# Kernel tuning notes

Measured on AMD Instinct MI355X. Metric: run time of the kernel, lower is better.

## Reference

```python
import jax, jax.numpy as jnp
import numpy as np


def setup_inputs() -> dict:
    key = jax.random.key(0)
    k1, k2, k3 = jax.random.split(key, 3)
    N, C, W = 32, 64, 4096
    F, WW = 128, 64
    x = jax.random.normal(k1, (N, C, W), dtype=jnp.float32)
    w = jax.random.normal(k2, (F, C, WW), dtype=jnp.float32)
    b = jax.random.normal(k3, (F,), dtype=jnp.float32)
    return {"x": x, "w": w, "b": b}


def reference(x, w, b):
    # FFT-based 1D cross-correlation (the original loops over N, F, C; here batched).
    # x: [N, C, W], w: [F, C, WW], b: [F]
    N, C, W = x.shape
    F, _, WW = w.shape
    pad = 0  # module's padding kwarg
    fftsize = 1 << int(np.ceil(np.log2(W + 2 * pad + WW - 1)))  # next_power2
    out_W = W + 2 * pad - WW + 1
    # rfft of zero-padded signals and filters
    xfft = jnp.fft.rfft(x, n=fftsize, axis=-1)          # [N, C, K]
    wfft = jnp.fft.rfft(w, n=fftsize, axis=-1)          # [F, C, K]
    # cross-correlation: multiply by conj of filter spectrum, sum over channels
    offt = jnp.einsum('nck,fck->nfk', xfft, jnp.conj(wfft))  # [N, F, K]
    out = jnp.fft.irfft(offt, n=fftsize, axis=-1)[..., :out_W]  # real part, first out_W samples
    return out + b[None, :, None]
```

## Files before the change

kernel.cpp:

```cpp
#include <hip/hip_runtime.h>


#define C_TOT    64
#define F_TOT    128
#define KW       64
#define OUT_W    4033
#define W_IN     4096
#define N_BATCH  32
#define T_BLK    256
#define XROWS    320
#define XSTR     40
#define WROW     40
#define TRS      260
#define CHUNK_SH 10240

typedef __attribute__((ext_vector_type(8))) short  short8;
typedef __attribute__((ext_vector_type(4))) float  floatx4;

__device__ inline unsigned short f32_to_bf16(float f) {
  unsigned int u = __float_as_uint(f);
  u += 0x7FFF + ((u >> 16) & 1);
  return (unsigned short)(u >> 16);
}

__device__ inline void async16(const unsigned short* g, unsigned short* l) {
  __builtin_amdgcn_global_load_lds(
      (const __attribute__((address_space(1))) unsigned int*)g,
      (__attribute__((address_space(3))) unsigned int*)l, 16, 0, 0);
}

__global__ __launch_bounds__(256) void conv1d_prep(
    const float* __restrict__ w, unsigned short* __restrict__ wsw) {
  int j = blockIdx.x * 256 + threadIdx.x;
  if (j < 64 * 2 * 128 * 8) {
    int c4  = (j & 7) * 4;
    int f   = (j >> 3) & 127;
    int tap = (j >> 10) & 1;
    int gi  = j >> 11;
    int k   = (gi & 15) + 32 * ((gi >> 4) & 1) + 16 * tap;
    int cg0 = (gi >> 5) * 32 + c4;
    const float* src = w + ((size_t)f * C_TOT + cg0) * KW + k;
    ushort4 o;
    o.x = f32_to_bf16(src[0 * KW]);
    o.y = f32_to_bf16(src[1 * KW]);
    o.z = f32_to_bf16(src[2 * KW]);
    o.w = f32_to_bf16(src[3 * KW]);
    *(ushort4*)&wsw[((size_t)(gi * 2 + tap) * 128 + f) * WROW + c4] = o;
  }
}

__global__ __launch_bounds__(256, 2) void conv1d_mfma(
    const float* __restrict__ x, const unsigned short* __restrict__ wsw,
    const float* __restrict__ b, float* __restrict__ out) {
  __shared__ union SM {
    unsigned short xt[XROWS * XSTR];
    float tr[32 * TRS];
  } sm;
  __shared__ unsigned short bls[2][CHUNK_SH];

  const int tid  = threadIdx.x;
  const int lane = tid & 63;
  const int q    = lane >> 4;
  const int col  = lane & 15;
  const int wv   = tid >> 6;
  const int n    = blockIdx.y;
  const int t0   = blockIdx.x * T_BLK;
  const int fh2  = wv & 1;
  const int th   = wv >> 1;

  const float* xrowb = x + (size_t)n * C_TOT * W_IN;

  floatx4 acc[8][4];
#pragma unroll
  for (int ms = 0; ms < 8; ++ms)
#pragma unroll
    for (int ft = 0; ft < 4; ++ft) acc[ms][ft] = (floatx4)0.0f;

#define STAGE_W(gi_, p_)                                                       \
  {                                                                            \
    const unsigned short* wb = wsw + (size_t)(gi_) * CHUNK_SH;                 \
    _Pragma("unroll")                                                          \
    for (int s = 0; s < 5; ++s) {                                              \
      int off = (s * 256 + tid) * 8;                                           \
      async16(wb + off, &bls[p_][off]);                                        \
    }                                                                          \
  }

#define STAGE_X(hc_)                                                           \
  {                                                                            \
    _Pragma("unroll")                                                          \
    for (int r = 0; r < 10; ++r) {                                             \
      int ti = (r % 5) * 64 + (tid & 63);                                      \
      int cl = ((r / 5) * 4 + (tid >> 6)) * 4;                                 \
      int gt = t0 + ti;                                                        \
      const float* src = xrowb + (size_t)((hc_) * 32 + cl) * W_IN + gt;        \
      float4 v = {0.f, 0.f, 0.f, 0.f};                                         \
      if (gt < W_IN) {                                                         \
        v.x = src[0];                                                          \
        v.y = src[W_IN];                                                       \
        v.z = src[2 * W_IN];                                                   \
        v.w = src[3 * W_IN];                                                   \
      }                                                                        \
      ushort4 o;                                                               \
      o.x = f32_to_bf16(v.x); o.y = f32_to_bf16(v.y);                          \
      o.z = f32_to_bf16(v.z); o.w = f32_to_bf16(v.w);                          \
      *(ushort4*)&sm.xt[ti * XSTR + cl] = o;                                   \
    }                                                                          \
  }

  STAGE_W(0, 0)
  STAGE_X(0)
  __syncthreads();

  for (int gi = 0; gi < 64; ++gi) {
    const int p = gi & 1;
    if (gi + 1 < 64) STAGE_W(gi + 1, p ^ 1)

    const int k1 = (gi & 15) + 32 * ((gi >> 4) & 1);
    const unsigned short* ap = &sm.xt[(128 * th + col + k1) * XSTR + q * 8];
    const unsigned short* bp = &bls[p][(fh2 * 64 + col) * WROW + q * 8];

    short8 A[9];
#pragma unroll
    for (int jj = 0; jj < 9; ++jj)
      A[jj] = *(const short8*)&ap[jj * 16 * XSTR];

#pragma unroll
    for (int tap = 0; tap < 2; ++tap) {
#pragma unroll
      for (int ft = 0; ft < 4; ++ft) {
        const short8 B = *(const short8*)&bp[(tap * 128 + ft * 16) * WROW];
#pragma unroll
        for (int ms = 0; ms < 8; ++ms)
          acc[ms][ft] = __builtin_amdgcn_mfma_f32_16x16x32_bf16(
              A[ms + tap], B, acc[ms][ft], 0, 0, 0);
      }
    }
    __syncthreads();
    if (gi == 31) {
      STAGE_X(1)
      __syncthreads();
    }
  }

  const int fs_w  = fh2 * 16 + col;
  const int fs_r  = tid >> 3;
  const int seg   = tid & 7;
  const int f_r   = (fs_r >> 4) * 64 + (fs_r & 15);
  const size_t ob = ((size_t)n * F_TOT) * OUT_W;

#pragma unroll
  for (int j = 0; j < 4; ++j) {
#pragma unroll
    for (int ms = 0; ms < 8; ++ms) {
      float4 vv;
      vv.x = acc[ms][j][0];
      vv.y = acc[ms][j][1];
      vv.z = acc[ms][j][2];
      vv.w = acc[ms][j][3];
      int tl = 128 * th + 16 * ms + 4 * q;
      *(float4*)&sm.tr[fs_w * TRS + tl] = vv;
    }
    __syncthreads();
    const int f = f_r + 16 * j;
    const float bias = b[f];
    const size_t obf = ob + (size_t)f * OUT_W;
#pragma unroll
    for (int j2 = 0; j2 < 8; ++j2) {
      int tl = seg * 4 + 32 * j2;
      float4 vv = *(const float4*)&sm.tr[fs_r * TRS + tl];
      vv.x += bias; vv.y += bias; vv.z += bias; vv.w += bias;
      int t = t0 + tl;
      if (t + 3 < OUT_W) {
        *(float4*)&out[obf + t] = vv;
      } else {
        float e[4] = {vv.x, vv.y, vv.z, vv.w};
#pragma unroll
        for (int u = 0; u < 4; ++u)
          if (t + u < OUT_W) out[obf + t + u] = e[u];
      }
    }
    __syncthreads();
  }
}

extern "C" void kernel_launch(void* const* d_in, const int* in_sizes, int n_in,
                              void* d_out, int out_size, void* d_ws, size_t ws_size,
                              hipStream_t stream) {
  const float* x = (const float*)d_in[0];
  const float* w = (const float*)d_in[1];
  const float* b = (const float*)d_in[2];
  float* out = (float*)d_out;

  unsigned short* wsw = (unsigned short*)d_ws;

  conv1d_prep<<<512, 256, 0, stream>>>(w, wsw);

  dim3 grid((OUT_W + T_BLK - 1) / T_BLK, N_BATCH);
  conv1d_mfma<<<grid, 256, 0, stream>>>(x, wsw, b, out);
}
```

Before: 194.7 us.

## Load pre-swizzled weight fragments directly from global into registers, drop LDS staging

```diff
diff --git a/kernel.cpp b/kernel.cpp
--- a/kernel.cpp
+++ b/kernel.cpp
@@ -10,9 +10,7 @@
 #define T_BLK    256
 #define XROWS    320
 #define XSTR     40
-#define WROW     40
 #define TRS      260
-#define CHUNK_SH 10240
 
 typedef __attribute__((ext_vector_type(8))) short  short8;
 typedef __attribute__((ext_vector_type(4))) float  floatx4;
@@ -23,29 +21,27 @@
   return (unsigned short)(u >> 16);
 }
 
-__device__ inline void async16(const unsigned short* g, unsigned short* l) {
-  __builtin_amdgcn_global_load_lds(
-      (const __attribute__((address_space(1))) unsigned int*)g,
-      (__attribute__((address_space(3))) unsigned int*)l, 16, 0, 0);
-}
-
 __global__ __launch_bounds__(256) void conv1d_prep(
     const float* __restrict__ w, unsigned short* __restrict__ wsw) {
   int j = blockIdx.x * 256 + threadIdx.x;
-  if (j < 64 * 2 * 128 * 8) {
-    int c4  = (j & 7) * 4;
-    int f   = (j >> 3) & 127;
+  if (j < 131072) {
+    int e4  = (j & 1) * 4;
+    int col = (j >> 1) & 15;
+    int q   = (j >> 5) & 3;
+    int ft  = (j >> 7) & 3;
+    int fh2 = (j >> 9) & 1;
     int tap = (j >> 10) & 1;
     int gi  = j >> 11;
     int k   = (gi & 15) + 32 * ((gi >> 4) & 1) + 16 * tap;
-    int cg0 = (gi >> 5) * 32 + c4;
-    const float* src = w + ((size_t)f * C_TOT + cg0) * KW + k;
+    int f   = fh2 * 64 + ft * 16 + col;
+    int c0  = (gi >> 5) * 32 + q * 8 + e4;
+    const float* src = w + ((size_t)f * C_TOT + c0) * KW + k;
     ushort4 o;
     o.x = f32_to_bf16(src[0 * KW]);
     o.y = f32_to_bf16(src[1 * KW]);
     o.z = f32_to_bf16(src[2 * KW]);
     o.w = f32_to_bf16(src[3 * KW]);
-    *(ushort4*)&wsw[((size_t)(gi * 2 + tap) * 128 + f) * WROW + c4] = o;
+    *(ushort4*)&wsw[(size_t)j * 4] = o;
   }
 }
 
@@ -56,7 +52,6 @@
     unsigned short xt[XROWS * XSTR];
     float tr[32 * TRS];
   } sm;
-  __shared__ unsigned short bls[2][CHUNK_SH];
 
   const int tid  = threadIdx.x;
   const int lane = tid & 63;
@@ -69,22 +64,13 @@
   const int th   = wv >> 1;
 
   const float* xrowb = x + (size_t)n * C_TOT * W_IN;
+  const short8* wf = (const short8*)wsw;
 
   floatx4 acc[8][4];
 #pragma unroll
   for (int ms = 0; ms < 8; ++ms)
 #pragma unroll
     for (int ft = 0; ft < 4; ++ft) acc[ms][ft] = (floatx4)0.0f;
-
-#define STAGE_W(gi_, p_)                                                       \
-  {                                                                            \
-    const unsigned short* wb = wsw + (size_t)(gi_) * CHUNK_SH;                 \
-    _Pragma("unroll")                                                          \
-    for (int s = 0; s < 5; ++s) {                                              \
-      int off = (s * 256 + tid) * 8;                                           \
-      async16(wb + off, &bls[p_][off]);                                        \
-    }                                                                          \
-  }
 
 #define STAGE_X(hc_)                                                           \
   {                                                                            \
@@ -108,40 +94,57 @@
     }                                                                          \
   }
 
-  STAGE_W(0, 0)
+#define BFRAG(gi_, tap_, ft_) \
+  wf[(size_t)(((gi_) * 2 + (tap_)) * 2 + fh2) * 256 + (ft_) * 64 + lane]
+
+#define BODY(gi_, Bt0_, Bn_)                                                   \
+  {                                                                            \
+    const int k1 = ((gi_) & 15) + 32 * (((gi_) >> 4) & 1);                     \
+    short8 Bt1[4];                                                             \
+    _Pragma("unroll")                                                          \
+    for (int ft = 0; ft < 4; ++ft) Bt1[ft] = BFRAG(gi_, 1, ft);                \
+    const unsigned short* ap = &sm.xt[(128 * th + col + k1) * XSTR + q * 8];   \
+    short8 A[9];                                                               \
+    _Pragma("unroll")                                                          \
+    for (int jj = 0; jj < 9; ++jj)                                             \
+      A[jj] = *(const short8*)&ap[jj * 16 * XSTR];                             \
+    if ((gi_) + 1 < 64) {                                                      \
+      _Pragma("unroll")                                                        \
+      for (int ft = 0; ft < 4; ++ft) Bn_[ft] = BFRAG((gi_) + 1, 0, ft);        \
+    }                                                                          \
+    __builtin_amdgcn_s_setprio(1);                                             \
+    _Pragma("unroll")                                                          \
+    for (int ft = 0; ft < 4; ++ft)                                             \
+      _Pragma("unroll")                                                        \
+      for (int ms = 0; ms < 8; ++ms)                                           \
+        acc[ms][ft] = __builtin_amdgcn_mfma_f32_16x16x32_bf16(                 \
+            A[ms], Bt0_[ft], acc[ms][ft], 0, 0, 0);                            \
+    _Pragma("unroll")                                                          \
+    for (int ft = 0; ft < 4; ++ft)                                             \
+      _Pragma("unroll")                                                        \
+      for (int ms = 0; ms < 8; ++ms)                                           \
+        acc[ms][ft] = __builtin_amdgcn_mfma_f32_16x16x32_bf16(                 \
+            A[ms + 1], Bt1[ft], acc[ms][ft], 0, 0, 0);                         \
+    __builtin_amdgcn_s_setprio(0);                                             \
+  }
+
   STAGE_X(0)
+  short8 B0[4], B1[4];
+#pragma unroll
+  for (int ft = 0; ft < 4; ++ft) B0[ft] = BFRAG(0, 0, ft);
   __syncthreads();
 
-  for (int gi = 0; gi < 64; ++gi) {
-    const int p = gi & 1;
-    if (gi + 1 < 64) STAGE_W(gi + 1, p ^ 1)
-
-    const int k1 = (gi & 15) + 32 * ((gi >> 4) & 1);
-    const unsigned short* ap = &sm.xt[(128 * th + col + k1) * XSTR + q * 8];
-    const unsigned short* bp = &bls[p][(fh2 * 64 + col) * WROW + q * 8];
-
-    short8 A[9];
-#pragma unroll
-    for (int jj = 0; jj < 9; ++jj)
-      A[jj] = *(const short8*)&ap[jj * 16 * XSTR];
-
-#pragma unroll
-    for (int tap = 0; tap < 2; ++tap) {
-#pragma unroll
-      for (int ft = 0; ft < 4; ++ft) {
-        const short8 B = *(const short8*)&bp[(tap * 128 + ft * 16) * WROW];
-#pragma unroll
-        for (int ms = 0; ms < 8; ++ms)
-          acc[ms][ft] = __builtin_amdgcn_mfma_f32_16x16x32_bf16(
-              A[ms + tap], B, acc[ms][ft], 0, 0, 0);
-      }
-    }
-    __syncthreads();
-    if (gi == 31) {
+  for (int g2 = 0; g2 < 32; ++g2) {
+    const int gi = 2 * g2;
+    BODY(gi, B0, B1)
+    BODY(gi + 1, B1, B0)
+    if (gi + 1 == 31) {
+      __syncthreads();
       STAGE_X(1)
       __syncthreads();
     }
   }
+  __syncthreads();
 
   const int fs_w  = fh2 * 16 + col;
   const int fs_r  = tid >> 3;
```

Measured after the change: 188.8 us. 1.03x faster.

## Switch to 32x32x16 MFMA with register-direct weight fragments and full-channel x staging

Applied to the files above, without the earlier changes.

```diff
diff --git a/kernel.cpp b/kernel.cpp
--- a/kernel.cpp
+++ b/kernel.cpp
@@ -9,13 +9,11 @@
 #define N_BATCH  32
 #define T_BLK    256
 #define XROWS    320
-#define XSTR     40
-#define WROW     40
+#define XSTR     72
 #define TRS      260
-#define CHUNK_SH 10240
 
-typedef __attribute__((ext_vector_type(8))) short  short8;
-typedef __attribute__((ext_vector_type(4))) float  floatx4;
+typedef __attribute__((ext_vector_type(8)))  short short8;
+typedef __attribute__((ext_vector_type(16))) float f32x16;
 
 __device__ inline unsigned short f32_to_bf16(float f) {
   unsigned int u = __float_as_uint(f);
@@ -23,29 +21,29 @@
   return (unsigned short)(u >> 16);
 }
 
-__device__ inline void async16(const unsigned short* g, unsigned short* l) {
-  __builtin_amdgcn_global_load_lds(
-      (const __attribute__((address_space(1))) unsigned int*)g,
-      (__attribute__((address_space(3))) unsigned int*)l, 16, 0, 0);
-}
-
 __global__ __launch_bounds__(256) void conv1d_prep(
     const float* __restrict__ w, unsigned short* __restrict__ wsw) {
   int j = blockIdx.x * 256 + threadIdx.x;
-  if (j < 64 * 2 * 128 * 8) {
-    int c4  = (j & 7) * 4;
-    int f   = (j >> 3) & 127;
-    int tap = (j >> 10) & 1;
-    int gi  = j >> 11;
-    int k   = (gi & 15) + 32 * ((gi >> 4) & 1) + 16 * tap;
-    int cg0 = (gi >> 5) * 32 + c4;
-    const float* src = w + ((size_t)f * C_TOT + cg0) * KW + k;
+  if (j < 131072) {
+    int e4    = (j & 1) * 4;
+    int lane  = (j >> 1) & 63;
+    int frag  = j >> 7;
+    int g16   = frag & 1;
+    int ftile = (frag >> 1) & 1;
+    int fh2   = (frag >> 2) & 1;
+    int tap   = (frag >> 3) & 1;
+    int k1    = (frag >> 4) & 31;
+    int hc    = (frag >> 9) & 1;
+    int k  = k1 + 32 * tap;
+    int f  = fh2 * 64 + ftile * 32 + (lane & 31);
+    int c0 = hc * 32 + g16 * 16 + (lane >> 5) * 8 + e4;
+    const float* src = w + ((size_t)f * C_TOT + c0) * KW + k;
     ushort4 o;
     o.x = f32_to_bf16(src[0 * KW]);
     o.y = f32_to_bf16(src[1 * KW]);
     o.z = f32_to_bf16(src[2 * KW]);
     o.w = f32_to_bf16(src[3 * KW]);
-    *(ushort4*)&wsw[((size_t)(gi * 2 + tap) * 128 + f) * WROW + c4] = o;
+    *(ushort4*)&wsw[(size_t)j * 4] = o;
   }
 }
 
@@ -54,121 +52,113 @@
     const float* __restrict__ b, float* __restrict__ out) {
   __shared__ union SM {
     unsigned short xt[XROWS * XSTR];
-    float tr[32 * TRS];
+    float tr[64 * TRS];
   } sm;
-  __shared__ unsigned short bls[2][CHUNK_SH];
 
-  const int tid  = threadIdx.x;
-  const int lane = tid & 63;
-  const int q    = lane >> 4;
-  const int col  = lane & 15;
-  const int wv   = tid >> 6;
-  const int n    = blockIdx.y;
-  const int t0   = blockIdx.x * T_BLK;
-  const int fh2  = wv & 1;
-  const int th   = wv >> 1;
+  const int tid   = threadIdx.x;
+  const int lane  = tid & 63;
+  const int row32 = lane & 31;
+  const int kg    = lane >> 5;
+  const int wv    = tid >> 6;
+  const int fh2   = wv & 1;
+  const int th    = wv >> 1;
+  const int n     = blockIdx.y;
+  const int t0    = blockIdx.x * T_BLK;
 
   const float* xrowb = x + (size_t)n * C_TOT * W_IN;
+  const short8* wf   = (const short8*)wsw;
 
-  floatx4 acc[8][4];
+  f32x16 acc[4][2];
 #pragma unroll
-  for (int ms = 0; ms < 8; ++ms)
+  for (int tt = 0; tt < 4; ++tt)
 #pragma unroll
-    for (int ft = 0; ft < 4; ++ft) acc[ms][ft] = (floatx4)0.0f;
+    for (int ft = 0; ft < 2; ++ft) acc[tt][ft] = (f32x16)0.0f;
 
-#define STAGE_W(gi_, p_)                                                       \
-  {                                                                            \
-    const unsigned short* wb = wsw + (size_t)(gi_) * CHUNK_SH;                 \
-    _Pragma("unroll")                                                          \
-    for (int s = 0; s < 5; ++s) {                                              \
-      int off = (s * 256 + tid) * 8;                                           \
-      async16(wb + off, &bls[p_][off]);                                        \
-    }                                                                          \
+#pragma unroll 4
+  for (int r = 0; r < 20; ++r) {
+    int jj  = r * 256 + tid;
+    int cl4 = (jj & 15) * 4;
+    int ti  = jj >> 4;
+    int gt  = t0 + ti;
+    const float* src = xrowb + (size_t)cl4 * W_IN + gt;
+    float4 v = {0.f, 0.f, 0.f, 0.f};
+    if (gt < W_IN) {
+      v.x = src[0];
+      v.y = src[W_IN];
+      v.z = src[2 * W_IN];
+      v.w = src[3 * W_IN];
+    }
+    ushort4 o;
+    o.x = f32_to_bf16(v.x); o.y = f32_to_bf16(v.y);
+    o.z = f32_to_bf16(v.z); o.w = f32_to_bf16(v.w);
+    *(ushort4*)&sm.xt[ti * XSTR + cl4] = o;
   }
-
-#define STAGE_X(hc_)                                                           \
-  {                                                                            \
-    _Pragma("unroll")                                                          \
-    for (int r = 0; r < 10; ++r) {                                             \
-      int ti = (r % 5) * 64 + (tid & 63);                                      \
-      int cl = ((r / 5) * 4 + (tid >> 6)) * 4;                                 \
-      int gt = t0 + ti;                                                        \
-      const float* src = xrowb + (size_t)((hc_) * 32 + cl) * W_IN + gt;        \
-      float4 v = {0.f, 0.f, 0.f, 0.f};                                         \
-      if (gt < W_IN) {                                                         \
-        v.x = src[0];                                                          \
-        v.y = src[W_IN];                                                       \
-        v.z = src[2 * W_IN];                                                   \
-        v.w = src[3 * W_IN];                                                   \
-      }                                                                        \
-      ushort4 o;                                                               \
-      o.x = f32_to_bf16(v.x); o.y = f32_to_bf16(v.y);                          \
-      o.z = f32_to_bf16(v.z); o.w = f32_to_bf16(v.w);                          \
-      *(ushort4*)&sm.xt[ti * XSTR + cl] = o;                                   \
-    }                                                                          \
-  }
-
-  STAGE_W(0, 0)
-  STAGE_X(0)
   __syncthreads();
 
-  for (int gi = 0; gi < 64; ++gi) {
-    const int p = gi & 1;
-    if (gi + 1 < 64) STAGE_W(gi + 1, p ^ 1)
+  for (int hc = 0; hc < 2; ++hc) {
+    for (int k1 = 0; k1 < 32; ++k1) {
+      const short8* fb = wf + ((size_t)((hc * 32 + k1) * 16 + fh2 * 4)) * 64 + lane;
+      short8 B[2][2][2];
+#pragma unroll
+      for (int g = 0; g < 2; ++g)
+#pragma unroll
+        for (int tap = 0; tap < 2; ++tap)
+#pragma unroll
+          for (int ft = 0; ft < 2; ++ft)
+            B[g][tap][ft] = fb[(tap * 8 + ft * 2 + g) * 64];
 
-    const int k1 = (gi & 15) + 32 * ((gi >> 4) & 1);
-    const unsigned short* ap = &sm.xt[(128 * th + col + k1) * XSTR + q * 8];
-    const unsigned short* bp = &bls[p][(fh2 * 64 + col) * WROW + q * 8];
+      const unsigned short* ap =
+          &sm.xt[(128 * th + k1 + row32) * XSTR + hc * 32 + kg * 8];
+      short8 A[2][5];
+#pragma unroll
+      for (int g = 0; g < 2; ++g)
+#pragma unroll
+        for (int jr = 0; jr < 5; ++jr)
+          A[g][jr] = *(const short8*)&ap[jr * 32 * XSTR + g * 16];
 
-    short8 A[9];
+      __builtin_amdgcn_s_setprio(1);
 #pragma unroll
-    for (int jj = 0; jj < 9; ++jj)
-      A[jj] = *(const short8*)&ap[jj * 16 * XSTR];
+      for (int g = 0; g < 2; ++g)
+#pragma unroll
+        for (int tap = 0; tap < 2; ++tap)
+#pragma unroll
+          for (int tt = 0; tt < 4; ++tt)
+#pragma unroll
+            for (int ft = 0; ft < 2; ++ft)
+              acc[tt][ft] = __builtin_amdgcn_mfma_f32_32x32x16_bf16(
+                  A[g][tt + tap], B[g][tap][ft], acc[tt][ft], 0, 0, 0);
+      __builtin_amdgcn_s_setprio(0);
+    }
+  }
+  __syncthreads();
+
+  const int slot_w = fh2 * 32 + row32;
+  const int s_r    = tid >> 2;
+  const int seg    = tid & 3;
+  const size_t ob  = ((size_t)n * F_TOT) * OUT_W;
 
 #pragma unroll
-    for (int tap = 0; tap < 2; ++tap) {
+  for (int jr = 0; jr < 2; ++jr) {
 #pragma unroll
-      for (int ft = 0; ft < 4; ++ft) {
-        const short8 B = *(const short8*)&bp[(tap * 128 + ft * 16) * WROW];
+    for (int tt = 0; tt < 4; ++tt)
 #pragma unroll
-        for (int ms = 0; ms < 8; ++ms)
-          acc[ms][ft] = __builtin_amdgcn_mfma_f32_16x16x32_bf16(
-              A[ms + tap], B, acc[ms][ft], 0, 0, 0);
+      for (int g = 0; g < 4; ++g) {
+        float4 vv;
+        vv.x = acc[tt][jr][4 * g + 0];
+        vv.y = acc[tt][jr][4 * g + 1];
+        vv.z = acc[tt][jr][4 * g + 2];
+        vv.w = acc[tt][jr][4 * g + 3];
+        int tl = 128 * th + 32 * tt + 8 * g + 4 * kg;
+        *(float4*)&sm.tr[slot_w * TRS + tl] = vv;
       }
-    }
     __syncthreads();
-    if (gi == 31) {
-      STAGE_X(1)
-      __syncthreads();
-    }
-  }
-
-  const int fs_w  = fh2 * 16 + col;
-  const int fs_r  = tid >> 3;
-  const int seg   = tid & 7;
-  const int f_r   = (fs_r >> 4) * 64 + (fs_r & 15);
-  const size_t ob = ((size_t)n * F_TOT) * OUT_W;
-
-#pragma unroll
-  for (int j = 0; j < 4; ++j) {
-#pragma unroll
-    for (int ms = 0; ms < 8; ++ms) {
-      float4 vv;
-      vv.x = acc[ms][j][0];
-      vv.y = acc[ms][j][1];
-      vv.z = acc[ms][j][2];
-      vv.w = acc[ms][j][3];
-      int tl = 128 * th + 16 * ms + 4 * q;
-      *(float4*)&sm.tr[fs_w * TRS + tl] = vv;
-    }
-    __syncthreads();
-    const int f = f_r + 16 * j;
+    const int f = (s_r >> 5) * 64 + jr * 32 + (s_r & 31);
     const float bias = b[f];
     const size_t obf = ob + (size_t)f * OUT_W;
 #pragma unroll
-    for (int j2 = 0; j2 < 8; ++j2) {
-      int tl = seg * 4 + 32 * j2;
-      float4 vv = *(const float4*)&sm.tr[fs_r * TRS + tl];
+    for (int j2 = 0; j2 < 16; ++j2) {
+      int tl = seg * 4 + 16 * j2;
+      float4 vv = *(const float4*)&sm.tr[s_r * TRS + tl];
       vv.x += bias; vv.y += bias; vv.z += bias; vv.w += bias;
       int t = t0 + tl;
       if (t + 3 < OUT_W) {
```

Result: slower. 215.5 us (+10.7%).

## Load weight fragments directly from global into registers, drop LDS weight staging

Applied to the files above, without the earlier changes.

```diff
diff --git a/kernel.cpp b/kernel.cpp
--- a/kernel.cpp
+++ b/kernel.cpp
@@ -10,9 +10,7 @@
 #define T_BLK    256
 #define XROWS    320
 #define XSTR     40
-#define WROW     40
 #define TRS      260
-#define CHUNK_SH 10240
 
 typedef __attribute__((ext_vector_type(8))) short  short8;
 typedef __attribute__((ext_vector_type(4))) float  floatx4;
@@ -23,29 +21,27 @@
   return (unsigned short)(u >> 16);
 }
 
-__device__ inline void async16(const unsigned short* g, unsigned short* l) {
-  __builtin_amdgcn_global_load_lds(
-      (const __attribute__((address_space(1))) unsigned int*)g,
-      (__attribute__((address_space(3))) unsigned int*)l, 16, 0, 0);
-}
-
 __global__ __launch_bounds__(256) void conv1d_prep(
     const float* __restrict__ w, unsigned short* __restrict__ wsw) {
   int j = blockIdx.x * 256 + threadIdx.x;
-  if (j < 64 * 2 * 128 * 8) {
-    int c4  = (j & 7) * 4;
-    int f   = (j >> 3) & 127;
+  if (j < 131072) {
+    int e4  = (j & 1) * 4;
+    int col = (j >> 1) & 15;
+    int q   = (j >> 5) & 3;
+    int ft  = (j >> 7) & 3;
+    int fh2 = (j >> 9) & 1;
     int tap = (j >> 10) & 1;
     int gi  = j >> 11;
     int k   = (gi & 15) + 32 * ((gi >> 4) & 1) + 16 * tap;
-    int cg0 = (gi >> 5) * 32 + c4;
-    const float* src = w + ((size_t)f * C_TOT + cg0) * KW + k;
+    int f   = fh2 * 64 + ft * 16 + col;
+    int c0  = (gi >> 5) * 32 + q * 8 + e4;
+    const float* src = w + ((size_t)f * C_TOT + c0) * KW + k;
     ushort4 o;
     o.x = f32_to_bf16(src[0 * KW]);
     o.y = f32_to_bf16(src[1 * KW]);
     o.z = f32_to_bf16(src[2 * KW]);
     o.w = f32_to_bf16(src[3 * KW]);
-    *(ushort4*)&wsw[((size_t)(gi * 2 + tap) * 128 + f) * WROW + c4] = o;
+    *(ushort4*)&wsw[(size_t)j * 4] = o;
   }
 }
 
@@ -56,7 +52,6 @@
     unsigned short xt[XROWS * XSTR];
     float tr[32 * TRS];
   } sm;
-  __shared__ unsigned short bls[2][CHUNK_SH];
 
   const int tid  = threadIdx.x;
   const int lane = tid & 63;
@@ -69,22 +64,13 @@
   const int th   = wv >> 1;
 
   const float* xrowb = x + (size_t)n * C_TOT * W_IN;
+  const short8* wp = (const short8*)wsw + fh2 * 256 + lane;
 
   floatx4 acc[8][4];
 #pragma unroll
   for (int ms = 0; ms < 8; ++ms)
 #pragma unroll
     for (int ft = 0; ft < 4; ++ft) acc[ms][ft] = (floatx4)0.0f;
-
-#define STAGE_W(gi_, p_)                                                       \
-  {                                                                            \
-    const unsigned short* wb = wsw + (size_t)(gi_) * CHUNK_SH;                 \
-    _Pragma("unroll")                                                          \
-    for (int s = 0; s < 5; ++s) {                                              \
-      int off = (s * 256 + tid) * 8;                                           \
-      async16(wb + off, &bls[p_][off]);                                        \
-    }                                                                          \
-  }
 
 #define STAGE_X(hc_)                                                           \
   {                                                                            \
@@ -108,40 +94,68 @@
     }                                                                          \
   }
 
-  STAGE_W(0, 0)
   STAGE_X(0)
+  short8 Bt0[4];
+#pragma unroll
+  for (int ft = 0; ft < 4; ++ft) Bt0[ft] = wp[ft * 64];
   __syncthreads();
 
   for (int gi = 0; gi < 64; ++gi) {
-    const int p = gi & 1;
-    if (gi + 1 < 64) STAGE_W(gi + 1, p ^ 1)
-
     const int k1 = (gi & 15) + 32 * ((gi >> 4) & 1);
+
+    short8 Bt1[4];
+#pragma unroll
+    for (int ft = 0; ft < 4; ++ft) Bt1[ft] = wp[512 + ft * 64];
+
     const unsigned short* ap = &sm.xt[(128 * th + col + k1) * XSTR + q * 8];
-    const unsigned short* bp = &bls[p][(fh2 * 64 + col) * WROW + q * 8];
-
-    short8 A[9];
-#pragma unroll
-    for (int jj = 0; jj < 9; ++jj)
-      A[jj] = *(const short8*)&ap[jj * 16 * XSTR];
-
-#pragma unroll
-    for (int tap = 0; tap < 2; ++tap) {
-#pragma unroll
-      for (int ft = 0; ft < 4; ++ft) {
-        const short8 B = *(const short8*)&bp[(tap * 128 + ft * 16) * WROW];
-#pragma unroll
-        for (int ms = 0; ms < 8; ++ms)
-          acc[ms][ft] = __builtin_amdgcn_mfma_f32_16x16x32_bf16(
-              A[ms + tap], B, acc[ms][ft], 0, 0, 0);
-      }
-    }
-    __syncthreads();
+
+    short8 As[3];
+    As[0] = *(const short8*)&ap[0];
+    As[1] = *(const short8*)&ap[1 * 16 * XSTR];
+    __builtin_amdgcn_s_setprio(1);
+#pragma unroll
+    for (int ms = 0; ms < 8; ++ms) {
+      if (ms < 6)
+        As[(ms + 2) % 3] = *(const short8*)&ap[(ms + 2) * 16 * XSTR];
+#pragma unroll
+      for (int ft = 0; ft < 4; ++ft)
+        acc[ms][ft] = __builtin_amdgcn_mfma_f32_16x16x32_bf16(
+            As[ms % 3], Bt0[ft], acc[ms][ft], 0, 0, 0);
+    }
+    __builtin_amdgcn_s_setprio(0);
+    __builtin_amdgcn_sched_barrier(0);
+
+    const short8* wn = (gi < 63) ? wp + 1024 : wp;
+    short8 Bn[4];
+#pragma unroll
+    for (int ft = 0; ft < 4; ++ft) Bn[ft] = wn[ft * 64];
+
+    short8 Az[3];
+    Az[1] = *(const short8*)&ap[1 * 16 * XSTR];
+    Az[2] = *(const short8*)&ap[2 * 16 * XSTR];
+    __builtin_amdgcn_s_setprio(1);
+#pragma unroll
+    for (int ms = 0; ms < 8; ++ms) {
+      if (ms < 6)
+        Az[ms % 3] = *(const short8*)&ap[(ms + 3) * 16 * XSTR];
+#pragma unroll
+      for (int ft = 0; ft < 4; ++ft)
+        acc[ms][ft] = __builtin_amdgcn_mfma_f32_16x16x32_bf16(
+            Az[(ms + 1) % 3], Bt1[ft], acc[ms][ft], 0, 0, 0);
+    }
+    __builtin_amdgcn_s_setprio(0);
+
+#pragma unroll
+    for (int ft = 0; ft < 4; ++ft) Bt0[ft] = Bn[ft];
+    wp += 1024;
+
     if (gi == 31) {
+      __syncthreads();
       STAGE_X(1)
       __syncthreads();
     }
   }
+  __syncthreads();
 
   const int fs_w  = fh2 * 16 + col;
   const int fs_r  = tid >> 3;
```

After: 185.8 us. 1.05x faster.
